# Performance work log

Hardware: AMD Instinct MI355X
Metric: run time of the kernel (lower is better)

## Reference

```python
import jax, jax.numpy as jnp
import numpy as np
import math

B, L, H, E, D = 4, 1024, 8, 64, 64


def setup_inputs() -> dict:
    key = jax.random.key(0)
    kq, kk, kv, ks = jax.random.split(key, 4)
    return {
        "queries": jax.random.normal(kq, (B, L, H, E), dtype=jnp.float32),
        "keys": jax.random.normal(kk, (B, L, H, E), dtype=jnp.float32),
        "values": jax.random.normal(kv, (B, L, H, D), dtype=jnp.float32),
        "sigma": jax.random.normal(ks, (B, L, H), dtype=jnp.float32),
    }


def reference(queries, keys, values, sigma):
    b, l, h, e = queries.shape
    scale = 1.0 / math.sqrt(e)

    # scores: [B, H, L, S]
    scores = jnp.einsum("blhe,bshe->bhls", queries, keys)

    # triangular causal mask (strict upper triangle -> -inf), applied BEFORE scaling
    causal = jnp.triu(jnp.ones((l, l), dtype=bool), k=1)  # [L, L]
    scores = jnp.where(causal[None, None], -jnp.inf, scores)
    attn = scale * scores

    # sigma branch: [B, L, H] -> [B, H, L], sigmoid/pow transform, broadcast over S
    sg = jax.nn.sigmoid(jnp.transpose(sigma, (0, 2, 1)) * 5.0) + 1e-5
    sg = jnp.power(3.0, sg) - 1.0          # [B, H, L]
    sg = sg[..., None]                      # [B, H, L, 1] (broadcast instead of tile)

    # Gaussian prior from |i - j| distances
    idx = jnp.arange(l, dtype=jnp.float32)
    dist = jnp.abs(idx[:, None] - idx[None, :])  # [L, L]
    prior = (1.0 / (math.sqrt(2.0 * math.pi) * sg)) * jnp.exp(-(dist ** 2) / (2.0 * sg ** 2))  # [B,H,L,L]

    series = jax.nn.softmax(attn, axis=-1)  # dropout rate 0.0 -> identity
    V = jnp.einsum("bhls,bshd->blhd", series, values)

    sigma_out = jnp.broadcast_to(sg, prior.shape)  # matches tf.tile semantics
    return (V, series, prior, sigma_out)
```

## Files before the change

### kernel.cpp

```cpp
#include <hip/hip_runtime.h>
#include <hip/hip_bf16.h>

#define NB 4
#define NL 1024
#define NH 8
#define NE 64
#define NPRIOR (NB * NH * NL)

typedef __bf16 bf16x8_t __attribute__((ext_vector_type(8)));
typedef __bf16 bf16x4_t __attribute__((ext_vector_type(4)));
typedef float f32x4_t __attribute__((ext_vector_type(4)));

__device__ __forceinline__ int kidx(int row, int col) {
    return (row << 6) + (col ^ ((row & 7) << 3));
}
__device__ __forceinline__ int pidx(int row, int col) {
    return (row << 10) + (col ^ ((row & 7) << 3));
}

#define BAR() do { asm volatile("s_waitcnt lgkmcnt(0)" ::: "memory"); \
                   __builtin_amdgcn_s_barrier();                      \
                   asm volatile("" ::: "memory"); } while (0)

__global__ __launch_bounds__(256) void fused_kernel(
    const float* __restrict__ Qg, const float* __restrict__ Kg,
    const float* __restrict__ Vg, const float* __restrict__ Sgm,
    float* __restrict__ outV, float* __restrict__ outSer,
    float* __restrict__ outP, float* __restrict__ outSig)
{
    __shared__ __bf16 Pl[32 * 1024];
    __shared__ __bf16 KV[64 * 64];
    __shared__ float rsum[4][16];
    __shared__ float rinvs[32];
    __shared__ float sgl[72], cstl[72], nil[72];

    const int bid = blockIdx.x;
    const int p  = bid & 31;
    const int jp = bid >> 5;
    const int h = p & 7, b = p >> 3;
    const int tid = threadIdx.x;
    const int lane = tid & 63, wave = tid >> 6;
    const int l16 = lane & 15, lq = lane >> 4;
    const int rg  = wave >> 1;
    const int nsb = (wave & 1) << 1;
    const int rowstride = NH * NE;

    const float* Qb = Qg + ((size_t)b * NL) * rowstride + h * NE;
    const float* Kb = Kg + ((size_t)b * NL) * rowstride + h * NE;
    const float* Vb = Vg + ((size_t)b * NL) * rowstride + h * NE;
    float* ser = outSer + ((size_t)p << 20);
    const float scale = 0.125f;

    if (tid < 72) {
        const int g = (bid << 6) + tid;
        if (g < NPRIOR) {
            const int i  = g & (NL - 1);
            const int ph = g >> 10;
            const float s   = Sgm[((size_t)(ph >> 3) * NL + i) * NH + (ph & 7)];
            const float sig = 1.f / (1.f + __expf(-5.f * s)) + 1e-5f;
            const float sg  = expm1f(sig * 1.0986122886681098f);
            sgl[tid]  = sg;
            cstl[tid] = 0.3989422804014327f / sg;
            nil[tid]  = -0.5f / (sg * sg);
        }
    }

    int prow = 0;
    auto emit4 = [&]() {
        #pragma unroll
        for (int c = 0; c < 4; ++c) {
            const int lr = prow + c;
            const int g  = (bid << 6) + lr;
            if (g < NPRIOR) {
                const int i  = g & (NL - 1);
                const int ph = g >> 10;
                const float sg  = sgl[lr];
                const float cst = cstl[lr];
                const float ni  = nil[lr];
                const size_t ob = ((size_t)ph << 20) + ((size_t)i << 10);
                const int j0 = tid << 2;
                const float fd = (float)(i - j0);
                f32x4_t pr;
                pr.x = cst * __expf(fd * fd * ni);
                const float f1 = fd - 1.f; pr.y = cst * __expf(f1 * f1 * ni);
                const float f2 = fd - 2.f; pr.z = cst * __expf(f2 * f2 * ni);
                const float f3 = fd - 3.f; pr.w = cst * __expf(f3 * f3 * ni);
                __builtin_nontemporal_store(pr, (f32x4_t*)(outP + ob + j0));
                f32x4_t sv = {sg, sg, sg, sg};
                __builtin_nontemporal_store(sv, (f32x4_t*)(outSig + ob + j0));
            }
        }
        prow += 4;
    };

    float4 preK[4], preV[4];
    auto loadT = [&](const float* base, int ct, float4 (&dst)[4]) {
        const float* src = base + ((size_t)(ct << 6)) * rowstride;
        #pragma unroll
        for (int it = 0; it < 4; ++it) {
            int g = tid + (it << 8);
            int row = g >> 4, c4 = (g & 15) << 2;
            dst[it] = *(const float4*)(src + (size_t)row * rowstride + c4);
        }
    };
    auto writeK = [&]() {
        #pragma unroll
        for (int it = 0; it < 4; ++it) {
            int g = tid + (it << 8);
            int row = g >> 4, c4 = (g & 15) << 2;
            bf16x4_t w;
            w[0] = (__bf16)preK[it].x; w[1] = (__bf16)preK[it].y;
            w[2] = (__bf16)preK[it].z; w[3] = (__bf16)preK[it].w;
            *(bf16x4_t*)(KV + kidx(row, c4)) = w;
        }
    };
    auto writeVt = [&]() {
        #pragma unroll
        for (int it = 0; it < 4; ++it) {
            int g = tid + (it << 8);
            int row = g >> 4, c4 = (g & 15) << 2;
            KV[kidx(c4 + 0, row)] = (__bf16)preV[it].x;
            KV[kidx(c4 + 1, row)] = (__bf16)preV[it].y;
            KV[kidx(c4 + 2, row)] = (__bf16)preV[it].z;
            KV[kidx(c4 + 3, row)] = (__bf16)preV[it].w;
        }
    };

    auto do_tile = [&](int t) {
        const int r0  = t << 5;
        const int nct = (t + 2) >> 1;

        loadT(Kb, 0, preK);
        loadT(Vb, 0, preV);

        BAR();
        #pragma unroll
        for (int it = 0; it < 2; ++it) {
            int g = tid + (it << 8);
            int row = g >> 4, c4 = (g & 15) << 2;
            float4 v = *(const float4*)(Qb + (size_t)(r0 + row) * rowstride + c4);
            bf16x4_t w;
            w[0] = (__bf16)v.x; w[1] = (__bf16)v.y;
            w[2] = (__bf16)v.z; w[3] = (__bf16)v.w;
            *(bf16x4_t*)(KV + kidx(row, c4)) = w;
        }
        BAR();
        bf16x8_t qf0, qf1;
        {
            int row = (rg << 4) + l16;
            qf0 = *(bf16x8_t*)(KV + kidx(row, lq << 3));
            qf1 = *(bf16x8_t*)(KV + kidx(row, 32 + (lq << 3)));
        }

        const int rloc0 = (rg << 4) + (lq << 2);
        const int ig0   = r0 + rloc0;

        float psum[4] = {0.f, 0.f, 0.f, 0.f};
        f32x4_t accO0 = {0.f, 0.f, 0.f, 0.f};
        f32x4_t accO1 = {0.f, 0.f, 0.f, 0.f};

        for (int ct = 0; ct < nct; ++ct) {
            BAR();
            writeK();
            if (ct + 1 < nct) loadT(Kb, ct + 1, preK);
            BAR();
            #pragma unroll
            for (int nn = 0; nn < 2; ++nn) {
                int ns = nsb + nn;
                int krow = (ns << 4) + l16;
                bf16x8_t k0 = *(bf16x8_t*)(KV + kidx(krow, lq << 3));
                bf16x8_t k1 = *(bf16x8_t*)(KV + kidx(krow, 32 + (lq << 3)));
                f32x4_t acc = {0.f, 0.f, 0.f, 0.f};
                acc = __builtin_amdgcn_mfma_f32_16x16x32_bf16(qf0, k0, acc, 0, 0, 0);
                acc = __builtin_amdgcn_mfma_f32_16x16x32_bf16(qf1, k1, acc, 0, 0, 0);
                int jg = (ct << 6) + (ns << 4) + l16;
                #pragma unroll
                for (int r = 0; r < 4; ++r) {
                    float e = (jg <= ig0 + r) ? __expf(acc[r] * scale) : 0.f;
                    psum[r] += e;
                    Pl[pidx(rloc0 + r, jg)] = (__bf16)e;
                }
            }
            BAR();
            writeVt();
            if (ct + 1 < nct) loadT(Vb, ct + 1, preV);
            BAR();
            #pragma unroll
            for (int ks = 0; ks < 2; ++ks) {
                bf16x8_t pa = *(bf16x8_t*)(Pl + pidx((rg << 4) + l16,
                                             (ct << 6) + (ks << 5) + (lq << 3)));
                bf16x8_t vb0 = *(bf16x8_t*)(KV + kidx((nsb << 4) + l16,
                                             (ks << 5) + (lq << 3)));
                accO0 = __builtin_amdgcn_mfma_f32_16x16x32_bf16(pa, vb0, accO0, 0, 0, 0);
                bf16x8_t vb1 = *(bf16x8_t*)(KV + kidx(((nsb + 1) << 4) + l16,
                                             (ks << 5) + (lq << 3)));
                accO1 = __builtin_amdgcn_mfma_f32_16x16x32_bf16(pa, vb1, accO1, 0, 0, 0);
            }
            emit4();
        }

        #pragma unroll
        for (int r = 0; r < 4; ++r) {
            float s = psum[r];
            s += __shfl_xor(s, 1);
            s += __shfl_xor(s, 2);
            s += __shfl_xor(s, 4);
            s += __shfl_xor(s, 8);
            psum[r] = s;
        }
        if (l16 == 0) {
            #pragma unroll
            for (int r = 0; r < 4; ++r) rsum[wave][(lq << 2) + r] = psum[r];
        }
        BAR();
        if (tid < 32) {
            int rgx = tid >> 4;
            float tot = rsum[rgx << 1][tid & 15] + rsum[(rgx << 1) | 1][tid & 15];
            rinvs[tid] = 1.f / tot;
        }
        BAR();

        #pragma unroll
        for (int r = 0; r < 4; ++r) {
            int rloc = rloc0 + r;
            float rv = rinvs[rloc];
            float* dst = outV + ((size_t)b * NL + r0 + rloc) * rowstride + h * NE;
            dst[(nsb << 4) + l16]       = accO0[r] * rv;
            dst[((nsb + 1) << 4) + l16] = accO1[r] * rv;
        }

        const int lim = nct << 6;
        #pragma unroll 2
        for (int rr = wave; rr < 32; rr += 4) {
            float rv = rinvs[rr];
            float* dst = ser + ((size_t)(r0 + rr) << 10);
            #pragma unroll
            for (int k = 0; k < 4; ++k) {
                int col = (lane << 2) + (k << 8);
                f32x4_t o;
                if (col < lim) {
                    bf16x4_t p4 = *(bf16x4_t*)(Pl + pidx(rr, col));
                    o.x = (float)p4[0] * rv;
                    o.y = (float)p4[1] * rv;
                    o.z = (float)p4[2] * rv;
                    o.w = (float)p4[3] * rv;
                } else {
                    o.x = 0.f; o.y = 0.f; o.z = 0.f; o.w = 0.f;
                }
                __builtin_nontemporal_store(o, (f32x4_t*)(dst + col));
            }
        }
    };

    do_tile(31 - jp);
    do_tile(jp);

    while (prow < 64) emit4();
}

extern "C" void kernel_launch(void* const* d_in, const int* in_sizes, int n_in,
                              void* d_out, int out_size, void* d_ws, size_t ws_size,
                              hipStream_t stream) {
    const float* Q  = (const float*)d_in[0];
    const float* K  = (const float*)d_in[1];
    const float* V  = (const float*)d_in[2];
    const float* Sg = (const float*)d_in[3];

    float* out      = (float*)d_out;
    float* outV     = out;
    float* outSer   = out + 2097152;
    float* outPrior = out + 35651584;
    float* outSig   = out + 69206016;

    hipLaunchKernelGGL(fused_kernel, dim3(512), dim3(256), 0, stream,
                       Q, K, V, Sg, outV, outSer, outPrior, outSig);
}
```

Measured before the change: 86.96 us.

## Load K fragments directly to registers and transpose QK MFMA to cut LDS staging

K tiles are now read from global memory straight into each lane's MFMA operand layout and converted to bf16 in registers, which removes the LDS write of K and one barrier per column tile. The QK^T MFMA operands are swapped so each lane holds four consecutive key columns for a single query row. This lets P be stored as one packed bf16x4 write and lets the row-sum reduction shrink to two cross-lane shuffles. The cost is redundant global loads of K across waves (each wave loads its own fragments, with less coalescing) and more registers held live.

```diff
diff --git a/kernel.cpp b/kernel.cpp
--- a/kernel.cpp
+++ b/kernel.cpp
@@ -93,25 +93,27 @@
         prow += 4;
     };
 
-    float4 preK[4], preV[4];
-    auto loadT = [&](const float* base, int ct, float4 (&dst)[4]) {
-        const float* src = base + ((size_t)(ct << 6)) * rowstride;
+    float4 kr[8];
+    auto loadK = [&](int ct) {
+        #pragma unroll
+        for (int nn = 0; nn < 2; ++nn) {
+            const float* row = Kb +
+                (size_t)((ct << 6) + ((nsb + nn) << 4) + l16) * rowstride;
+            kr[nn * 4 + 0] = *(const float4*)(row + (lq << 3));
+            kr[nn * 4 + 1] = *(const float4*)(row + (lq << 3) + 4);
+            kr[nn * 4 + 2] = *(const float4*)(row + 32 + (lq << 3));
+            kr[nn * 4 + 3] = *(const float4*)(row + 32 + (lq << 3) + 4);
+        }
+    };
+
+    float4 preV[4];
+    auto loadV = [&](int ct) {
+        const float* src = Vb + ((size_t)(ct << 6)) * rowstride;
         #pragma unroll
         for (int it = 0; it < 4; ++it) {
             int g = tid + (it << 8);
             int row = g >> 4, c4 = (g & 15) << 2;
-            dst[it] = *(const float4*)(src + (size_t)row * rowstride + c4);
-        }
-    };
-    auto writeK = [&]() {
-        #pragma unroll
-        for (int it = 0; it < 4; ++it) {
-            int g = tid + (it << 8);
-            int row = g >> 4, c4 = (g & 15) << 2;
-            bf16x4_t w;
-            w[0] = (__bf16)preK[it].x; w[1] = (__bf16)preK[it].y;
-            w[2] = (__bf16)preK[it].z; w[3] = (__bf16)preK[it].w;
-            *(bf16x4_t*)(KV + kidx(row, c4)) = w;
+            preV[it] = *(const float4*)(src + (size_t)row * rowstride + c4);
         }
     };
     auto writeVt = [&]() {
@@ -130,8 +132,8 @@
         const int r0  = t << 5;
         const int nct = (t + 2) >> 1;
 
-        loadT(Kb, 0, preK);
-        loadT(Vb, 0, preV);
+        loadK(0);
+        loadV(0);
 
         BAR();
         #pragma unroll
@@ -152,38 +154,47 @@
             qf1 = *(bf16x8_t*)(KV + kidx(row, 32 + (lq << 3)));
         }
 
+        const int qloc = (rg << 4) + l16;
+        const int qg   = r0 + qloc;
         const int rloc0 = (rg << 4) + (lq << 2);
-        const int ig0   = r0 + rloc0;
-
-        float psum[4] = {0.f, 0.f, 0.f, 0.f};
+
+        float psum = 0.f;
         f32x4_t accO0 = {0.f, 0.f, 0.f, 0.f};
         f32x4_t accO1 = {0.f, 0.f, 0.f, 0.f};
 
         for (int ct = 0; ct < nct; ++ct) {
             BAR();
-            writeK();
-            if (ct + 1 < nct) loadT(Kb, ct + 1, preK);
-            BAR();
+            writeVt();
+            if (ct + 1 < nct) loadV(ct + 1);
             #pragma unroll
             for (int nn = 0; nn < 2; ++nn) {
-                int ns = nsb + nn;
-                int krow = (ns << 4) + l16;
-                bf16x8_t k0 = *(bf16x8_t*)(KV + kidx(krow, lq << 3));
-                bf16x8_t k1 = *(bf16x8_t*)(KV + kidx(krow, 32 + (lq << 3)));
+                bf16x8_t a0, a1;
+                {
+                    float4 p0 = kr[nn * 4 + 0], p1 = kr[nn * 4 + 1];
+                    float4 p2 = kr[nn * 4 + 2], p3 = kr[nn * 4 + 3];
+                    a0[0] = (__bf16)p0.x; a0[1] = (__bf16)p0.y;
+                    a0[2] = (__bf16)p0.z; a0[3] = (__bf16)p0.w;
+                    a0[4] = (__bf16)p1.x; a0[5] = (__bf16)p1.y;
+                    a0[6] = (__bf16)p1.z; a0[7] = (__bf16)p1.w;
+                    a1[0] = (__bf16)p2.x; a1[1] = (__bf16)p2.y;
+                    a1[2] = (__bf16)p2.z; a1[3] = (__bf16)p2.w;
+                    a1[4] = (__bf16)p3.x; a1[5] = (__bf16)p3.y;
+                    a1[6] = (__bf16)p3.z; a1[7] = (__bf16)p3.w;
+                }
                 f32x4_t acc = {0.f, 0.f, 0.f, 0.f};
-                acc = __builtin_amdgcn_mfma_f32_16x16x32_bf16(qf0, k0, acc, 0, 0, 0);
-                acc = __builtin_amdgcn_mfma_f32_16x16x32_bf16(qf1, k1, acc, 0, 0, 0);
-                int jg = (ct << 6) + (ns << 4) + l16;
+                acc = __builtin_amdgcn_mfma_f32_16x16x32_bf16(a0, qf0, acc, 0, 0, 0);
+                acc = __builtin_amdgcn_mfma_f32_16x16x32_bf16(a1, qf1, acc, 0, 0, 0);
+                const int jbase = (ct << 6) + ((nsb + nn) << 4) + (lq << 2);
+                bf16x4_t pw;
                 #pragma unroll
                 for (int r = 0; r < 4; ++r) {
-                    float e = (jg <= ig0 + r) ? __expf(acc[r] * scale) : 0.f;
-                    psum[r] += e;
-                    Pl[pidx(rloc0 + r, jg)] = (__bf16)e;
+                    float e = (jbase + r <= qg) ? __expf(acc[r] * scale) : 0.f;
+                    psum += e;
+                    pw[r] = (__bf16)e;
                 }
-            }
-            BAR();
-            writeVt();
-            if (ct + 1 < nct) loadT(Vb, ct + 1, preV);
+                *(bf16x4_t*)(Pl + pidx(qloc, jbase)) = pw;
+            }
+            if (ct + 1 < nct) loadK(ct + 1);
             BAR();
             #pragma unroll
             for (int ks = 0; ks < 2; ++ks) {
@@ -199,18 +210,11 @@
             emit4();
         }
 
-        #pragma unroll
-        for (int r = 0; r < 4; ++r) {
-            float s = psum[r];
-            s += __shfl_xor(s, 1);
-            s += __shfl_xor(s, 2);
-            s += __shfl_xor(s, 4);
-            s += __shfl_xor(s, 8);
-            psum[r] = s;
-        }
-        if (l16 == 0) {
-            #pragma unroll
-            for (int r = 0; r < 4; ++r) rsum[wave][(lq << 2) + r] = psum[r];
+        {
+            float s = psum;
+            s += __shfl_xor(s, 16);
+            s += __shfl_xor(s, 32);
+            if (lane < 16) rsum[wave][l16] = s;
         }
         BAR();
         if (tid < 32) {
```

New measurement: 87.26 us. About the same (+0.3%).

## Split attention into score and PV passes and interleave output stores with compute

Applied to the files above, without the earlier changes.

The per-tile loop is split into two passes. The first computes scores and exponentials for all key tiles, then the row sums. The second does the P·V MFMAs and writes normalized series slabs to global memory as each column block finishes, instead of in one final loop. Zero-fill stores for the masked region and prior/sigma row emission (now two rows at a time) are spread across both passes so memory writes overlap with compute. This adds an extra reduction barrier before PV, and the zero slabs and prior rows now depend on exact iteration counts to cover every output.

```diff
diff --git a/kernel.cpp b/kernel.cpp
--- a/kernel.cpp
+++ b/kernel.cpp
@@ -32,7 +32,7 @@
     __shared__ __bf16 KV[64 * 64];
     __shared__ float rsum[4][16];
     __shared__ float rinvs[32];
-    __shared__ float sgl[72], cstl[72], nil[72];
+    __shared__ float sgl[64], cstl[64], nil[64];
 
     const int bid = blockIdx.x;
     const int p  = bid & 31;
@@ -51,27 +51,28 @@
     float* ser = outSer + ((size_t)p << 20);
     const float scale = 0.125f;
 
-    if (tid < 72) {
-        const int g = (bid << 6) + tid;
-        if (g < NPRIOR) {
-            const int i  = g & (NL - 1);
-            const int ph = g >> 10;
-            const float s   = Sgm[((size_t)(ph >> 3) * NL + i) * NH + (ph & 7)];
-            const float sig = 1.f / (1.f + __expf(-5.f * s)) + 1e-5f;
-            const float sg  = expm1f(sig * 1.0986122886681098f);
-            sgl[tid]  = sg;
-            cstl[tid] = 0.3989422804014327f / sg;
-            nil[tid]  = -0.5f / (sg * sg);
-        }
+    const int srow = tid >> 3;
+    const int scol = (tid & 7) << 3;
+
+    if (tid < 64) {
+        const int g  = (bid << 6) + tid;
+        const int i  = g & (NL - 1);
+        const int ph = g >> 10;
+        const float s   = Sgm[((size_t)(ph >> 3) * NL + i) * NH + (ph & 7)];
+        const float sig = 1.f / (1.f + __expf(-5.f * s)) + 1e-5f;
+        const float sg  = expm1f(sig * 1.0986122886681098f);
+        sgl[tid]  = sg;
+        cstl[tid] = 0.3989422804014327f / sg;
+        nil[tid]  = -0.5f / (sg * sg);
     }
 
     int prow = 0;
-    auto emit4 = [&]() {
-        #pragma unroll
-        for (int c = 0; c < 4; ++c) {
-            const int lr = prow + c;
-            const int g  = (bid << 6) + lr;
-            if (g < NPRIOR) {
+    auto emit2 = [&]() {
+        if (prow < 64) {
+            #pragma unroll
+            for (int c = 0; c < 2; ++c) {
+                const int lr = prow + c;
+                const int g  = (bid << 6) + lr;
                 const int i  = g & (NL - 1);
                 const int ph = g >> 10;
                 const float sg  = sgl[lr];
@@ -89,8 +90,25 @@
                 f32x4_t sv = {sg, sg, sg, sg};
                 __builtin_nontemporal_store(sv, (f32x4_t*)(outSig + ob + j0));
             }
-        }
-        prow += 4;
+            prow += 2;
+        }
+    };
+
+    const int tA = 31 - jp, tB = jp;
+    const int nctA = (tA + 2) >> 1, nctB = (tB + 2) >> 1;
+    const int tailA = 16 - nctA;
+    int zs = 0;
+    auto zslab = [&]() {
+        if (zs < 15) {
+            int t_, c_;
+            if (zs < tailA) { t_ = tA; c_ = nctA + zs; }
+            else            { t_ = tB; c_ = nctB + (zs - tailA); }
+            float* dst = ser + ((size_t)((t_ << 5) + srow) << 10) + (c_ << 6) + scol;
+            f32x4_t z = {0.f, 0.f, 0.f, 0.f};
+            __builtin_nontemporal_store(z, (f32x4_t*)dst);
+            __builtin_nontemporal_store(z, (f32x4_t*)(dst + 4));
+            ++zs;
+        }
     };
 
     float4 preK[4], preV[4];
@@ -181,6 +199,33 @@
                     Pl[pidx(rloc0 + r, jg)] = (__bf16)e;
                 }
             }
+            zslab();
+            emit2();
+        }
+
+        #pragma unroll
+        for (int r = 0; r < 4; ++r) {
+            float s = psum[r];
+            s += __shfl_xor(s, 1);
+            s += __shfl_xor(s, 2);
+            s += __shfl_xor(s, 4);
+            s += __shfl_xor(s, 8);
+            psum[r] = s;
+        }
+        if (l16 == 0) {
+            #pragma unroll
+            for (int r = 0; r < 4; ++r) rsum[wave][(lq << 2) + r] = psum[r];
+        }
+        BAR();
+        if (tid < 32) {
+            int rgx = tid >> 4;
+            float tot = rsum[rgx << 1][tid & 15] + rsum[(rgx << 1) | 1][tid & 15];
+            rinvs[tid] = 1.f / tot;
+        }
+        BAR();
+
+        loadT(Vb, 0, preV);
+        for (int ct = 0; ct < nct; ++ct) {
             BAR();
             writeVt();
             if (ct + 1 < nct) loadT(Vb, ct + 1, preV);
@@ -196,29 +241,20 @@
                                              (ks << 5) + (lq << 3)));
                 accO1 = __builtin_amdgcn_mfma_f32_16x16x32_bf16(pa, vb1, accO1, 0, 0, 0);
             }
-            emit4();
-        }
-
-        #pragma unroll
-        for (int r = 0; r < 4; ++r) {
-            float s = psum[r];
-            s += __shfl_xor(s, 1);
-            s += __shfl_xor(s, 2);
-            s += __shfl_xor(s, 4);
-            s += __shfl_xor(s, 8);
-            psum[r] = s;
-        }
-        if (l16 == 0) {
-            #pragma unroll
-            for (int r = 0; r < 4; ++r) rsum[wave][(lq << 2) + r] = psum[r];
-        }
-        BAR();
-        if (tid < 32) {
-            int rgx = tid >> 4;
-            float tot = rsum[rgx << 1][tid & 15] + rsum[(rgx << 1) | 1][tid & 15];
-            rinvs[tid] = 1.f / tot;
-        }
-        BAR();
+            {
+                bf16x8_t p8 = *(bf16x8_t*)(Pl + pidx(srow, (ct << 6) + scol));
+                const float rv = rinvs[srow];
+                float* dst = ser + ((size_t)(r0 + srow) << 10) + (ct << 6) + scol;
+                f32x4_t o0, o1;
+                o0.x = (float)p8[0] * rv; o0.y = (float)p8[1] * rv;
+                o0.z = (float)p8[2] * rv; o0.w = (float)p8[3] * rv;
+                o1.x = (float)p8[4] * rv; o1.y = (float)p8[5] * rv;
+                o1.z = (float)p8[6] * rv; o1.w = (float)p8[7] * rv;
+                __builtin_nontemporal_store(o0, (f32x4_t*)dst);
+                __builtin_nontemporal_store(o1, (f32x4_t*)(dst + 4));
+            }
+            emit2();
+        }
 
         #pragma unroll
         for (int r = 0; r < 4; ++r) {
@@ -228,34 +264,13 @@
             dst[(nsb << 4) + l16]       = accO0[r] * rv;
             dst[((nsb + 1) << 4) + l16] = accO1[r] * rv;
         }
-
-        const int lim = nct << 6;
-        #pragma unroll 2
-        for (int rr = wave; rr < 32; rr += 4) {
-            float rv = rinvs[rr];
-            float* dst = ser + ((size_t)(r0 + rr) << 10);
-            #pragma unroll
-            for (int k = 0; k < 4; ++k) {
-                int col = (lane << 2) + (k << 8);
-                f32x4_t o;
-                if (col < lim) {
-                    bf16x4_t p4 = *(bf16x4_t*)(Pl + pidx(rr, col));
-                    o.x = (float)p4[0] * rv;
-                    o.y = (float)p4[1] * rv;
-                    o.z = (float)p4[2] * rv;
-                    o.w = (float)p4[3] * rv;
-                } else {
-                    o.x = 0.f; o.y = 0.f; o.z = 0.f; o.w = 0.f;
-                }
-                __builtin_nontemporal_store(o, (f32x4_t*)(dst + col));
-            }
-        }
-    };
-
-    do_tile(31 - jp);
-    do_tile(jp);
-
-    while (prow < 64) emit4();
+    };
+
+    do_tile(tA);
+    do_tile(tB);
+
+    while (zs < 15) zslab();
+    while (prow < 64) emit2();
 }
 
 extern "C" void kernel_launch(void* const* d_in, const int* in_sizes, int n_in,
```

After: 133.7 us. 1.54x slower.

## Halve query tile to 16 rows and double grid to 1024 blocks

Applied to the files above, without the earlier changes.

Shrinks each block's query tile from 32 to 16 rows, so every wave owns one 16-column slice of S and D instead of two. The grid doubles to 1024 blocks, and the LDS for the probability buffer halves, which allows a launch-bounds occupancy hint of 3 blocks per CU. The aim is more parallelism and better latency hiding for a store-bound kernel. In exchange, K and V tiles are reloaded more often per query row, and each block does less MFMA work per barrier.

```diff
diff --git a/kernel.cpp b/kernel.cpp
--- a/kernel.cpp
+++ b/kernel.cpp
@@ -22,17 +22,17 @@
                    __builtin_amdgcn_s_barrier();                      \
                    asm volatile("" ::: "memory"); } while (0)
 
-__global__ __launch_bounds__(256) void fused_kernel(
+__global__ __launch_bounds__(256, 3) void fused_kernel(
     const float* __restrict__ Qg, const float* __restrict__ Kg,
     const float* __restrict__ Vg, const float* __restrict__ Sgm,
     float* __restrict__ outV, float* __restrict__ outSer,
     float* __restrict__ outP, float* __restrict__ outSig)
 {
-    __shared__ __bf16 Pl[32 * 1024];
+    __shared__ __bf16 Pl[16 * 1024];
     __shared__ __bf16 KV[64 * 64];
     __shared__ float rsum[4][16];
-    __shared__ float rinvs[32];
-    __shared__ float sgl[72], cstl[72], nil[72];
+    __shared__ float rinvs[16];
+    __shared__ float sgl[32], cstl[32], nil[32];
 
     const int bid = blockIdx.x;
     const int p  = bid & 31;
@@ -41,8 +41,7 @@
     const int tid = threadIdx.x;
     const int lane = tid & 63, wave = tid >> 6;
     const int l16 = lane & 15, lq = lane >> 4;
-    const int rg  = wave >> 1;
-    const int nsb = (wave & 1) << 1;
+    const int nc  = wave;
     const int rowstride = NH * NE;
 
     const float* Qb = Qg + ((size_t)b * NL) * rowstride + h * NE;
@@ -51,27 +50,25 @@
     float* ser = outSer + ((size_t)p << 20);
     const float scale = 0.125f;
 
-    if (tid < 72) {
-        const int g = (bid << 6) + tid;
-        if (g < NPRIOR) {
-            const int i  = g & (NL - 1);
-            const int ph = g >> 10;
-            const float s   = Sgm[((size_t)(ph >> 3) * NL + i) * NH + (ph & 7)];
-            const float sig = 1.f / (1.f + __expf(-5.f * s)) + 1e-5f;
-            const float sg  = expm1f(sig * 1.0986122886681098f);
-            sgl[tid]  = sg;
-            cstl[tid] = 0.3989422804014327f / sg;
-            nil[tid]  = -0.5f / (sg * sg);
-        }
+    if (tid < 32) {
+        const int g  = (bid << 5) + tid;
+        const int i  = g & (NL - 1);
+        const int ph = g >> 10;
+        const float s   = Sgm[((size_t)(ph >> 3) * NL + i) * NH + (ph & 7)];
+        const float sig = 1.f / (1.f + __expf(-5.f * s)) + 1e-5f;
+        const float sg  = expm1f(sig * 1.0986122886681098f);
+        sgl[tid]  = sg;
+        cstl[tid] = 0.3989422804014327f / sg;
+        nil[tid]  = -0.5f / (sg * sg);
     }
 
     int prow = 0;
-    auto emit4 = [&]() {
-        #pragma unroll
-        for (int c = 0; c < 4; ++c) {
-            const int lr = prow + c;
-            const int g  = (bid << 6) + lr;
-            if (g < NPRIOR) {
+    auto emit2 = [&]() {
+        if (prow < 32) {
+            #pragma unroll
+            for (int c = 0; c < 2; ++c) {
+                const int lr = prow + c;
+                const int g  = (bid << 5) + lr;
                 const int i  = g & (NL - 1);
                 const int ph = g >> 10;
                 const float sg  = sgl[lr];
@@ -89,8 +86,8 @@
                 f32x4_t sv = {sg, sg, sg, sg};
                 __builtin_nontemporal_store(sv, (f32x4_t*)(outSig + ob + j0));
             }
-        }
-        prow += 4;
+            prow += 2;
+        }
     };
 
     float4 preK[4], preV[4];
@@ -127,17 +124,15 @@
     };
 
     auto do_tile = [&](int t) {
-        const int r0  = t << 5;
-        const int nct = (t + 2) >> 1;
+        const int r0  = t << 4;
+        const int nct = (t >> 2) + 1;
 
         loadT(Kb, 0, preK);
         loadT(Vb, 0, preV);
 
         BAR();
-        #pragma unroll
-        for (int it = 0; it < 2; ++it) {
-            int g = tid + (it << 8);
-            int row = g >> 4, c4 = (g & 15) << 2;
+        {
+            int row = tid >> 4, c4 = (tid & 15) << 2;
             float4 v = *(const float4*)(Qb + (size_t)(r0 + row) * rowstride + c4);
             bf16x4_t w;
             w[0] = (__bf16)v.x; w[1] = (__bf16)v.y;
@@ -147,33 +142,29 @@
         BAR();
         bf16x8_t qf0, qf1;
         {
-            int row = (rg << 4) + l16;
-            qf0 = *(bf16x8_t*)(KV + kidx(row, lq << 3));
-            qf1 = *(bf16x8_t*)(KV + kidx(row, 32 + (lq << 3)));
-        }
-
-        const int rloc0 = (rg << 4) + (lq << 2);
+            qf0 = *(bf16x8_t*)(KV + kidx(l16, lq << 3));
+            qf1 = *(bf16x8_t*)(KV + kidx(l16, 32 + (lq << 3)));
+        }
+
+        const int rloc0 = lq << 2;
         const int ig0   = r0 + rloc0;
 
         float psum[4] = {0.f, 0.f, 0.f, 0.f};
-        f32x4_t accO0 = {0.f, 0.f, 0.f, 0.f};
-        f32x4_t accO1 = {0.f, 0.f, 0.f, 0.f};
+        f32x4_t accO = {0.f, 0.f, 0.f, 0.f};
 
         for (int ct = 0; ct < nct; ++ct) {
             BAR();
             writeK();
             if (ct + 1 < nct) loadT(Kb, ct + 1, preK);
             BAR();
-            #pragma unroll
-            for (int nn = 0; nn < 2; ++nn) {
-                int ns = nsb + nn;
-                int krow = (ns << 4) + l16;
+            {
+                int krow = (nc << 4) + l16;
                 bf16x8_t k0 = *(bf16x8_t*)(KV + kidx(krow, lq << 3));
                 bf16x8_t k1 = *(bf16x8_t*)(KV + kidx(krow, 32 + (lq << 3)));
                 f32x4_t acc = {0.f, 0.f, 0.f, 0.f};
                 acc = __builtin_amdgcn_mfma_f32_16x16x32_bf16(qf0, k0, acc, 0, 0, 0);
                 acc = __builtin_amdgcn_mfma_f32_16x16x32_bf16(qf1, k1, acc, 0, 0, 0);
-                int jg = (ct << 6) + (ns << 4) + l16;
+                int jg = (ct << 6) + (nc << 4) + l16;
                 #pragma unroll
                 for (int r = 0; r < 4; ++r) {
                     float e = (jg <= ig0 + r) ? __expf(acc[r] * scale) : 0.f;
@@ -187,16 +178,13 @@
             BAR();
             #pragma unroll
             for (int ks = 0; ks < 2; ++ks) {
-                bf16x8_t pa = *(bf16x8_t*)(Pl + pidx((rg << 4) + l16,
+                bf16x8_t pa = *(bf16x8_t*)(Pl + pidx(l16,
                                              (ct << 6) + (ks << 5) + (lq << 3)));
-                bf16x8_t vb0 = *(bf16x8_t*)(KV + kidx((nsb << 4) + l16,
+                bf16x8_t vb = *(bf16x8_t*)(KV + kidx((nc << 4) + l16,
                                              (ks << 5) + (lq << 3)));
-                accO0 = __builtin_amdgcn_mfma_f32_16x16x32_bf16(pa, vb0, accO0, 0, 0, 0);
-                bf16x8_t vb1 = *(bf16x8_t*)(KV + kidx(((nsb + 1) << 4) + l16,
-                                             (ks << 5) + (lq << 3)));
-                accO1 = __builtin_amdgcn_mfma_f32_16x16x32_bf16(pa, vb1, accO1, 0, 0, 0);
-            }
-            emit4();
+                accO = __builtin_amdgcn_mfma_f32_16x16x32_bf16(pa, vb, accO, 0, 0, 0);
+            }
+            emit2();
         }
 
         #pragma unroll
@@ -213,10 +201,9 @@
             for (int r = 0; r < 4; ++r) rsum[wave][(lq << 2) + r] = psum[r];
         }
         BAR();
-        if (tid < 32) {
-            int rgx = tid >> 4;
-            float tot = rsum[rgx << 1][tid & 15] + rsum[(rgx << 1) | 1][tid & 15];
-            rinvs[tid] = 1.f / tot;
+        if (tid < 16) {
+            rinvs[tid] = 1.f / (rsum[0][tid] + rsum[1][tid] +
+                                rsum[2][tid] + rsum[3][tid]);
         }
         BAR();
 
@@ -225,13 +212,12 @@
             int rloc = rloc0 + r;
             float rv = rinvs[rloc];
             float* dst = outV + ((size_t)b * NL + r0 + rloc) * rowstride + h * NE;
-            dst[(nsb << 4) + l16]       = accO0[r] * rv;
-            dst[((nsb + 1) << 4) + l16] = accO1[r] * rv;
+            dst[(nc << 4) + l16] = accO[r] * rv;
         }
 
         const int lim = nct << 6;
-        #pragma unroll 2
-        for (int rr = wave; rr < 32; rr += 4) {
+        #pragma unroll
+        for (int rr = wave; rr < 16; rr += 4) {
             float rv = rinvs[rr];
             float* dst = ser + ((size_t)(r0 + rr) << 10);
             #pragma unroll
@@ -252,10 +238,10 @@
         }
     };
 
-    do_tile(31 - jp);
+    do_tile(63 - jp);
     do_tile(jp);
 
-    while (prow < 64) emit4();
+    while (prow < 32) emit2();
 }
 
 extern "C" void kernel_launch(void* const* d_in, const int* in_sizes, int n_in,
@@ -272,6 +258,6 @@
     float* outPrior = out + 35651584;
     float* outSig   = out + 69206016;
 
-    hipLaunchKernelGGL(fused_kernel, dim3(512), dim3(256), 0, stream,
+    hipLaunchKernelGGL(fused_kernel, dim3(1024), dim3(256), 0, stream,
                        Q, K, V, Sg, outV, outSer, outPrior, outSig);
 }
```

Measured after the change: 85.39 us. About the same (-1.8%).
